# Kernel optimization log

Measured on AMD Instinct MI355X. Metric: run time of the kernel, lower is better.

## Reference

```python
import jax, jax.numpy as jnp
import numpy as np

CONFUSED_PAIRS = [(1, 2), (3, 4), (5, 6)]
NUM_CLASSES = 13
MARGIN = 0.5
IGNORE_INDEX = -100
BIG = 1e9  # finite sentinel instead of +/-inf (keeps grads clean)
EPS = 1e-12  # matches F.normalize eps

_conf_np = np.zeros((NUM_CLASSES, NUM_CLASSES), dtype=bool)
for _a, _b in CONFUSED_PAIRS:
    _conf_np[_a, _b] = True
    _conf_np[_b, _a] = True
CONF = jnp.asarray(_conf_np)  # [C, C] symmetric confused-class table


def setup_inputs() -> dict:
    key = jax.random.key(0)
    k1, k2 = jax.random.split(key)
    embeddings = jax.random.normal(k1, (16, 512, 256), dtype=jnp.float32)
    labels = jax.random.randint(k2, (16, 512), 0, 13, dtype=jnp.int64)
    return {"embeddings": embeddings, "labels": labels}


def reference(embeddings, labels):
    B, S, H = embeddings.shape
    e = embeddings.reshape(-1, H)                      # [N, H]
    lab = labels.reshape(-1)                           # [N]
    N = e.shape[0]

    valid = lab != IGNORE_INDEX                        # [N]
    # L2 normalize (F.normalize: divide by norm clamped to eps)
    norm = jnp.linalg.norm(e, axis=1, keepdims=True)
    e = e / jnp.maximum(norm, EPS)

    sim = e @ e.T                                      # [N, N] cosine sims

    lab_c = jnp.clip(lab, 0, NUM_CLASSES - 1)          # safe gather index
    # anchor label participates in some confused pair, and anchor is valid
    anchor_ok = valid & CONF[lab_c].any(axis=1)        # [N]

    same = lab[:, None] == lab[None, :]                # [N, N]
    eye = jnp.eye(N, dtype=bool)
    pos_mask = same & valid[None, :] & ~eye            # positives: same class, not self
    neg_mask = CONF[lab_c[:, None], lab_c[None, :]] & valid[None, :]  # confused-class negatives

    has_pos = pos_mask.any(axis=1)
    has_neg = neg_mask.any(axis=1)
    count_mask = anchor_ok & has_pos & has_neg         # [N] anchors contributing a triplet

    hardest_pos = jnp.min(jnp.where(pos_mask, sim, BIG), axis=1)   # [N]
    hardest_neg = jnp.max(jnp.where(neg_mask, sim, -BIG), axis=1)  # [N]

    triplet = jax.nn.relu(MARGIN + hardest_neg - hardest_pos)
    triplet = jnp.where(count_mask, triplet, 0.0)

    num_triplets = count_mask.sum()
    loss = triplet.sum() / jnp.maximum(num_triplets, 1).astype(triplet.dtype)
    return jnp.where(num_triplets > 0, loss, 0.0)
```

## Files before the change

### kernel.cpp

```cpp
#include <hip/hip_runtime.h>
#include <math.h>

#define Hdim    256
#define NMAX    8192
#define NCLS    13
#define NPADMAX (NMAX + NCLS * 32)
#define NBLK    32
#define WLMAX   264
#define NSPLIT  12
#define WPB     4
#define BIGV    1e9f
#define MARGIN  0.5f

typedef __attribute__((ext_vector_type(8))) short bf16x8;
typedef __attribute__((ext_vector_type(4))) float f32x4;

struct WS {
    unsigned short ebf[NPADMAX][Hdim];
    unsigned hpK[NPADMAX];
    unsigned hnK[NPADMAX];
    int labG[NPADMAX];
    int gpos[NMAX];
    int blockHist[NBLK][NCLS];
    int blockBase[NBLK][NCLS];
    int S[NCLS + 1];
    int n[NCLS];
    int wl_a[WLMAX];
    int wl_c[WLMAX];
    int T;
};

__device__ inline unsigned short f2bf(float f) {
    unsigned u = __float_as_uint(f);
    return (unsigned short)((u + 0x7fffu + ((u >> 16) & 1u)) >> 16);
}
__device__ inline unsigned fkey(float f) {
    unsigned u = __float_as_uint(f);
    return (u & 0x80000000u) ? ~u : (u | 0x80000000u);
}
__device__ inline float funkey(unsigned k) {
    unsigned u = (k & 0x80000000u) ? (k & 0x7fffffffu) : ~k;
    return __uint_as_float(u);
}

__global__ __launch_bounds__(256) void hist_init_kernel(const int* __restrict__ lab,
                                                        WS* ws, int N) {
    __shared__ int h[NCLS];
    int tid = threadIdx.x, b = blockIdx.x;
    if (tid < NCLS) h[tid] = 0;
    __syncthreads();
    for (int i = b * 256 + tid; i < N; i += NBLK * 256) {
        int l = lab[i];
        if (l >= 0 && l < NCLS) atomicAdd(&h[l], 1);
    }
    __syncthreads();
    if (tid < NCLS) ws->blockHist[b][tid] = h[tid];
    for (int idx = b * 256 + tid; idx < NPADMAX; idx += NBLK * 256) {
        ws->hpK[idx] = 0xFFFFFFFFu;
        ws->hnK[idx] = 0u;
        ws->labG[idx] = -1;
    }
}

__global__ __launch_bounds__(256) void plan_kernel(WS* ws) {
    __shared__ int sn[NCLS];
    int tid = threadIdx.x;
    if (tid < NCLS) {
        int s = 0;
        for (int b = 0; b < NBLK; ++b) s += ws->blockHist[b][tid];
        sn[tid] = s; ws->n[tid] = s;
    }
    __syncthreads();
    if (tid == 0) {
        int acc = 0;
        for (int c = 0; c < NCLS; ++c) { ws->S[c] = acc; acc += ((sn[c] + 31) >> 5) << 5; }
        ws->S[NCLS] = acc;
    }
    __syncthreads();
    if (tid < NCLS) {
        int base = ws->S[tid];
        for (int b = 0; b < NBLK; ++b) { ws->blockBase[b][tid] = base; base += ws->blockHist[b][tid]; }
    }
    if (tid == 0) {
        int T = 0;
        for (int c = 1; c <= 6; ++c) {
            int nt = (sn[c] + 31) >> 5;
            for (int k = 0; k < nt; ++k) { ws->wl_a[T] = ws->S[c] + 32 * k; ws->wl_c[T] = c; ++T; }
        }
        ws->T = T;
    }
}

__global__ __launch_bounds__(256) void rank_kernel(const int* __restrict__ lab,
                                                   WS* ws, int N) {
    __shared__ int cur[NCLS];
    int tid = threadIdx.x, b = blockIdx.x;
    if (tid < NCLS) cur[tid] = ws->blockBase[b][tid];
    __syncthreads();
    for (int i = b * 256 + tid; i < N; i += NBLK * 256) {
        int l = lab[i];
        int g = -1;
        if (l >= 0 && l < NCLS) g = atomicAdd(&cur[l], 1);
        ws->gpos[i] = g;
        if (g >= 0) ws->labG[g] = l;
    }
}

__global__ __launch_bounds__(256) void norm_gather_kernel(const float* __restrict__ in,
                                                          WS* ws, int N) {
    int row = blockIdx.x * 4 + (threadIdx.x >> 6);
    if (row >= N) return;
    int lane = threadIdx.x & 63;
    int g = ws->gpos[row];
    float4 v = ((const float4*)(in + (size_t)row * Hdim))[lane];
    float ss = v.x*v.x + v.y*v.y + v.z*v.z + v.w*v.w;
    #pragma unroll
    for (int off = 32; off >= 1; off >>= 1) ss += __shfl_xor(ss, off);
    float sc = 1.0f / fmaxf(sqrtf(ss), 1e-12f);
    ushort4 o;
    o.x = f2bf(v.x * sc); o.y = f2bf(v.y * sc);
    o.z = f2bf(v.z * sc); o.w = f2bf(v.w * sc);
    if (g >= 0) ((ushort4*)(&ws->ebf[g][0]))[lane] = o;
}

__global__ __launch_bounds__(256) void sim_kernel(WS* ws) {
    const int wave = threadIdx.x >> 6;
    const int lane = threadIdx.x & 63;
    const int col  = lane & 15;
    const int quad = lane >> 4;
    const int wid  = blockIdx.x * WPB + wave;
    const int tileIdx = wid / NSPLIT;
    const int split   = wid % NSPLIT;
    if (tileIdx >= ws->T) return;

    const int aBase = ws->wl_a[tileIdx];
    const int c     = ws->wl_c[tileIdx];
    const int p     = ((c - 1) ^ 1) + 1;
    const int posS = ws->S[c],  posPadE = ws->S[c + 1], posRealE = posS + ws->n[c];
    const int negS = ws->S[p],  negPadE = ws->S[p + 1], negRealE = negS + ws->n[p];
    const int nPosT = (posPadE - posS) >> 4;
    const int nT    = nPosT + ((negPadE - negS) >> 4);

    const unsigned short* ebf = &ws->ebf[0][0];

    bf16x8 afrag[2][8];
    #pragma unroll
    for (int t2 = 0; t2 < 2; ++t2) {
        const unsigned short* rp = ebf + (size_t)(aBase + t2 * 16 + col) * Hdim + quad * 8;
        #pragma unroll
        for (int ks = 0; ks < 8; ++ks)
            afrag[t2][ks] = *(const bf16x8*)(rp + ks * 32);
    }

    float runMin[2][4], runMax[2][4];
    #pragma unroll
    for (int t2 = 0; t2 < 2; ++t2)
        #pragma unroll
        for (int r = 0; r < 4; ++r) { runMin[t2][r] = BIGV; runMax[t2][r] = -BIGV; }

    auto j0Of = [&](int t) -> int {
        return (t < nPosT) ? (posS + (t << 4)) : (negS + ((t - nPosT) << 4));
    };
    bf16x8 b0[8], b1[8];
    auto loadB = [&](bf16x8 (&bf)[8], int t) {
        const unsigned short* rp = ebf + (size_t)(j0Of(t) + col) * Hdim + quad * 8;
        #pragma unroll
        for (int ks = 0; ks < 8; ++ks)
            bf[ks] = *(const bf16x8*)(rp + ks * 32);
    };
    auto computeT = [&](bf16x8 (&bf)[8], int t) {
        int j0 = j0Of(t);
        bool isPos = t < nPosT;
        int realE = isPos ? posRealE : negRealE;
        bool valid = (j0 + col) < realE;
        #pragma unroll
        for (int t2 = 0; t2 < 2; ++t2) {
            f32x4 acc = {0.f, 0.f, 0.f, 0.f};
            #pragma unroll
            for (int ks = 0; ks < 8; ++ks)
                acc = __builtin_amdgcn_mfma_f32_16x16x32_bf16(afrag[t2][ks], bf[ks], acc, 0, 0, 0);
            if (isPos) {
                #pragma unroll
                for (int r = 0; r < 4; ++r)
                    runMin[t2][r] = fminf(runMin[t2][r], valid ? acc[r] : BIGV);
            } else {
                #pragma unroll
                for (int r = 0; r < 4; ++r)
                    runMax[t2][r] = fmaxf(runMax[t2][r], valid ? acc[r] : -BIGV);
            }
        }
    };

    int nIter = (nT > split) ? ((nT - split + NSPLIT - 1) / NSPLIT) : 0;
    int t = split, i = 0;
    if (nIter > 0) loadB(b0, t);
    while (i + 2 <= nIter) {
        loadB(b1, t + NSPLIT);
        computeT(b0, t);
        if (i + 2 < nIter) loadB(b0, t + 2 * NSPLIT);
        computeT(b1, t + NSPLIT);
        t += 2 * NSPLIT; i += 2;
    }
    if (i < nIter) computeT(b0, t);

    #pragma unroll
    for (int t2 = 0; t2 < 2; ++t2)
        #pragma unroll
        for (int r = 0; r < 4; ++r) {
            float mn = runMin[t2][r], mx = runMax[t2][r];
            #pragma unroll
            for (int off = 1; off < 16; off <<= 1) {
                mn = fminf(mn, __shfl_xor(mn, off));
                mx = fmaxf(mx, __shfl_xor(mx, off));
            }
            if (col == 0) {
                int a = aBase + t2 * 16 + quad * 4 + r;
                if (mn < 1e8f)  atomicMin(&ws->hpK[a], fkey(mn));
                if (mx > -1e8f) atomicMax(&ws->hnK[a], fkey(mx));
            }
        }
}

__global__ __launch_bounds__(1024) void finalize_kernel(WS* ws, float* __restrict__ out) {
    __shared__ int ncls[NCLS];
    if (threadIdx.x < NCLS) ncls[threadIdx.x] = ws->n[threadIdx.x];
    __syncthreads();
    float sum = 0.f; int cnt = 0;
    for (int g = threadIdx.x; g < NPADMAX; g += 1024) {
        int l = ws->labG[g];
        if (l >= 1 && l <= 6) {
            int p = ((l - 1) ^ 1) + 1;
            if (ncls[l] >= 2 && ncls[p] >= 1) {
                float hp = funkey(ws->hpK[g]);
                float hn = funkey(ws->hnK[g]);
                float tr = MARGIN + hn - hp;
                if (tr > 0.f) sum += tr;
                cnt += 1;
            }
        }
    }
    #pragma unroll
    for (int off = 32; off >= 1; off >>= 1) {
        sum += __shfl_xor(sum, off);
        cnt += __shfl_xor(cnt, off);
    }
    __shared__ float ssum[16]; __shared__ int scnt[16];
    int w = threadIdx.x >> 6, lane = threadIdx.x & 63;
    if (lane == 0) { ssum[w] = sum; scnt[w] = cnt; }
    __syncthreads();
    if (threadIdx.x == 0) {
        float ts = 0.f; int tc = 0;
        #pragma unroll
        for (int k = 0; k < 16; ++k) { ts += ssum[k]; tc += scnt[k]; }
        out[0] = (tc > 0) ? ts / (float)tc : 0.f;
    }
}

extern "C" void kernel_launch(void* const* d_in, const int* in_sizes, int n_in,
                              void* d_out, int out_size, void* d_ws, size_t ws_size,
                              hipStream_t stream) {
    const float* emb = (const float*)d_in[0];
    const int*   lab = (const int*)d_in[1];
    int N = in_sizes[1];
    WS* ws = (WS*)d_ws;

    hist_init_kernel<<<NBLK, 256, 0, stream>>>(lab, ws, N);
    plan_kernel<<<1, 256, 0, stream>>>(ws);
    rank_kernel<<<NBLK, 256, 0, stream>>>(lab, ws, N);
    norm_gather_kernel<<<(N + 3) / 4, 256, 0, stream>>>(emb, ws, N);
    sim_kernel<<<(WLMAX * NSPLIT + WPB - 1) / WPB, 256, 0, stream>>>(ws);
    finalize_kernel<<<1, 1024, 0, stream>>>(ws, (float*)d_out);
}
```

Before: 103.8 us.

## Merge histogram/plan/rank into one kernel and fuse finalize into sim via last-block

Collapses the histogram, planning and ranking kernels into a single one-block kernel that only tracks classes 1-6. Normalization now skips rows with no confused class, and the finalize reduction runs inside the last finishing block of the sim kernel, found with an atomic done counter. NSPLIT rises from 12 to 16. This cuts launches from six to three and skips embedding rows that never contribute. The trade-offs are a single-block serial pass over the labels, and a norm_gather grid of N/16 that assumes N is a multiple of 16.

```diff
diff --git a/kernel.cpp b/kernel.cpp
--- a/kernel.cpp
+++ b/kernel.cpp
@@ -4,11 +4,11 @@
 #define Hdim    256
 #define NMAX    8192
 #define NCLS    13
-#define NPADMAX (NMAX + NCLS * 32)
-#define NBLK    32
+#define NPADMAX (NMAX + 6 * 32)
 #define WLMAX   264
-#define NSPLIT  12
+#define NSPLIT  16
 #define WPB     4
+#define SIMGRID ((WLMAX * NSPLIT) / WPB)
 #define BIGV    1e9f
 #define MARGIN  0.5f
 
@@ -21,13 +21,12 @@
     unsigned hnK[NPADMAX];
     int labG[NPADMAX];
     int gpos[NMAX];
-    int blockHist[NBLK][NCLS];
-    int blockBase[NBLK][NCLS];
-    int S[NCLS + 1];
-    int n[NCLS];
+    int S[8];
+    int n[8];
     int wl_a[WLMAX];
     int wl_c[WLMAX];
     int T;
+    unsigned done;
 };
 
 __device__ inline unsigned short f2bf(float f) {
@@ -43,75 +42,56 @@
     return __uint_as_float(u);
 }
 
-__global__ __launch_bounds__(256) void hist_init_kernel(const int* __restrict__ lab,
-                                                        WS* ws, int N) {
-    __shared__ int h[NCLS];
-    int tid = threadIdx.x, b = blockIdx.x;
-    if (tid < NCLS) h[tid] = 0;
-    __syncthreads();
-    for (int i = b * 256 + tid; i < N; i += NBLK * 256) {
+__global__ __launch_bounds__(1024) void plan_kernel(const int* __restrict__ lab,
+                                                    WS* ws, int N) {
+    __shared__ int h[8];
+    __shared__ int S[8];
+    __shared__ int cur[8];
+    const int tid = threadIdx.x;
+    if (tid < 8) h[tid] = 0;
+    __syncthreads();
+    for (int i = tid; i < N; i += 1024) {
         int l = lab[i];
-        if (l >= 0 && l < NCLS) atomicAdd(&h[l], 1);
-    }
-    __syncthreads();
-    if (tid < NCLS) ws->blockHist[b][tid] = h[tid];
-    for (int idx = b * 256 + tid; idx < NPADMAX; idx += NBLK * 256) {
-        ws->hpK[idx] = 0xFFFFFFFFu;
-        ws->hnK[idx] = 0u;
-        ws->labG[idx] = -1;
-    }
-}
-
-__global__ __launch_bounds__(256) void plan_kernel(WS* ws) {
-    __shared__ int sn[NCLS];
-    int tid = threadIdx.x;
-    if (tid < NCLS) {
-        int s = 0;
-        for (int b = 0; b < NBLK; ++b) s += ws->blockHist[b][tid];
-        sn[tid] = s; ws->n[tid] = s;
+        if (l >= 1 && l <= 6) atomicAdd(&h[l], 1);
     }
     __syncthreads();
     if (tid == 0) {
         int acc = 0;
-        for (int c = 0; c < NCLS; ++c) { ws->S[c] = acc; acc += ((sn[c] + 31) >> 5) << 5; }
-        ws->S[NCLS] = acc;
-    }
-    __syncthreads();
-    if (tid < NCLS) {
-        int base = ws->S[tid];
-        for (int b = 0; b < NBLK; ++b) { ws->blockBase[b][tid] = base; base += ws->blockHist[b][tid]; }
-    }
-    if (tid == 0) {
+        for (int c = 1; c <= 6; ++c) { S[c] = acc; acc += ((h[c] + 31) >> 5) << 5; }
+        S[7] = acc;
         int T = 0;
         for (int c = 1; c <= 6; ++c) {
-            int nt = (sn[c] + 31) >> 5;
-            for (int k = 0; k < nt; ++k) { ws->wl_a[T] = ws->S[c] + 32 * k; ws->wl_c[T] = c; ++T; }
+            int nt = (h[c] + 31) >> 5;
+            for (int k = 0; k < nt; ++k) { ws->wl_a[T] = S[c] + 32 * k; ws->wl_c[T] = c; ++T; }
         }
         ws->T = T;
-    }
-}
-
-__global__ __launch_bounds__(256) void rank_kernel(const int* __restrict__ lab,
-                                                   WS* ws, int N) {
-    __shared__ int cur[NCLS];
-    int tid = threadIdx.x, b = blockIdx.x;
-    if (tid < NCLS) cur[tid] = ws->blockBase[b][tid];
-    __syncthreads();
-    for (int i = b * 256 + tid; i < N; i += NBLK * 256) {
+        ws->done = 0u;
+        for (int c = 0; c < 8; ++c) { ws->n[c] = h[c]; ws->S[c] = S[c]; }
+        ws->S[7] = S[7];
+    }
+    __syncthreads();
+    const int SEnd = S[7];
+    for (int g = tid; g < SEnd; g += 1024) {
+        ws->hpK[g] = 0xFFFFFFFFu;
+        ws->hnK[g] = 0u;
+        ws->labG[g] = -1;
+    }
+    if (tid < 8) cur[tid] = S[tid];
+    __syncthreads();
+    for (int i = tid; i < N; i += 1024) {
         int l = lab[i];
         int g = -1;
-        if (l >= 0 && l < NCLS) g = atomicAdd(&cur[l], 1);
+        if (l >= 1 && l <= 6) { g = atomicAdd(&cur[l], 1); ws->labG[g] = l; }
         ws->gpos[i] = g;
-        if (g >= 0) ws->labG[g] = l;
-    }
-}
-
-__global__ __launch_bounds__(256) void norm_gather_kernel(const float* __restrict__ in,
-                                                          WS* ws, int N) {
-    int row = blockIdx.x * 4 + (threadIdx.x >> 6);
-    if (row >= N) return;
+    }
+}
+
+__global__ __launch_bounds__(1024) void norm_gather_kernel(const float* __restrict__ in,
+                                                           WS* ws) {
+    int row  = blockIdx.x * 16 + (threadIdx.x >> 6);
     int lane = threadIdx.x & 63;
     int g = ws->gpos[row];
+    if (g < 0) return;
     float4 v = ((const float4*)(in + (size_t)row * Hdim))[lane];
     float ss = v.x*v.x + v.y*v.y + v.z*v.z + v.w*v.w;
     #pragma unroll
@@ -120,10 +100,10 @@
     ushort4 o;
     o.x = f2bf(v.x * sc); o.y = f2bf(v.y * sc);
     o.z = f2bf(v.z * sc); o.w = f2bf(v.w * sc);
-    if (g >= 0) ((ushort4*)(&ws->ebf[g][0]))[lane] = o;
-}
-
-__global__ __launch_bounds__(256) void sim_kernel(WS* ws) {
+    ((ushort4*)(&ws->ebf[g][0]))[lane] = o;
+}
+
+__global__ __launch_bounds__(256) void sim_kernel(WS* ws, float* __restrict__ out) {
     const int wave = threadIdx.x >> 6;
     const int lane = threadIdx.x & 63;
     const int col  = lane & 15;
@@ -131,104 +111,119 @@
     const int wid  = blockIdx.x * WPB + wave;
     const int tileIdx = wid / NSPLIT;
     const int split   = wid % NSPLIT;
-    if (tileIdx >= ws->T) return;
-
-    const int aBase = ws->wl_a[tileIdx];
-    const int c     = ws->wl_c[tileIdx];
-    const int p     = ((c - 1) ^ 1) + 1;
-    const int posS = ws->S[c],  posPadE = ws->S[c + 1], posRealE = posS + ws->n[c];
-    const int negS = ws->S[p],  negPadE = ws->S[p + 1], negRealE = negS + ws->n[p];
-    const int nPosT = (posPadE - posS) >> 4;
-    const int nT    = nPosT + ((negPadE - negS) >> 4);
-
-    const unsigned short* ebf = &ws->ebf[0][0];
-
-    bf16x8 afrag[2][8];
-    #pragma unroll
-    for (int t2 = 0; t2 < 2; ++t2) {
-        const unsigned short* rp = ebf + (size_t)(aBase + t2 * 16 + col) * Hdim + quad * 8;
-        #pragma unroll
-        for (int ks = 0; ks < 8; ++ks)
-            afrag[t2][ks] = *(const bf16x8*)(rp + ks * 32);
-    }
-
-    float runMin[2][4], runMax[2][4];
-    #pragma unroll
-    for (int t2 = 0; t2 < 2; ++t2)
-        #pragma unroll
-        for (int r = 0; r < 4; ++r) { runMin[t2][r] = BIGV; runMax[t2][r] = -BIGV; }
-
-    auto j0Of = [&](int t) -> int {
-        return (t < nPosT) ? (posS + (t << 4)) : (negS + ((t - nPosT) << 4));
-    };
-    bf16x8 b0[8], b1[8];
-    auto loadB = [&](bf16x8 (&bf)[8], int t) {
-        const unsigned short* rp = ebf + (size_t)(j0Of(t) + col) * Hdim + quad * 8;
-        #pragma unroll
-        for (int ks = 0; ks < 8; ++ks)
-            bf[ks] = *(const bf16x8*)(rp + ks * 32);
-    };
-    auto computeT = [&](bf16x8 (&bf)[8], int t) {
-        int j0 = j0Of(t);
-        bool isPos = t < nPosT;
-        int realE = isPos ? posRealE : negRealE;
-        bool valid = (j0 + col) < realE;
+
+    if (tileIdx < ws->T) {
+        const int aBase = ws->wl_a[tileIdx];
+        const int c     = ws->wl_c[tileIdx];
+        const int p     = ((c - 1) ^ 1) + 1;
+        const int posS = ws->S[c], posRealE = posS + ws->n[c];
+        const int negS = ws->S[p], negRealE = negS + ws->n[p];
+        const int nPosT = (ws->S[c + 1] - posS) >> 4;
+        const int nT    = nPosT + ((((p == c + 1) ? ws->S[p + 1] : ws->S[p])
+                                    - negS) >> 4);
+        const int nNegT = ((ws->S[p + 1]) - negS) >> 4;
+        const int nTT = nPosT + nNegT;
+
+        const unsigned short* ebf = &ws->ebf[0][0];
+
+        bf16x8 afrag[2][8];
         #pragma unroll
         for (int t2 = 0; t2 < 2; ++t2) {
-            f32x4 acc = {0.f, 0.f, 0.f, 0.f};
+            const unsigned short* rp = ebf + (size_t)(aBase + t2 * 16 + col) * Hdim + quad * 8;
             #pragma unroll
             for (int ks = 0; ks < 8; ++ks)
-                acc = __builtin_amdgcn_mfma_f32_16x16x32_bf16(afrag[t2][ks], bf[ks], acc, 0, 0, 0);
-            if (isPos) {
+                afrag[t2][ks] = *(const bf16x8*)(rp + ks * 32);
+        }
+
+        float runMin[2][4], runMax[2][4];
+        #pragma unroll
+        for (int t2 = 0; t2 < 2; ++t2)
+            #pragma unroll
+            for (int r = 0; r < 4; ++r) { runMin[t2][r] = BIGV; runMax[t2][r] = -BIGV; }
+
+        auto j0Of = [&](int t) -> int {
+            return (t < nPosT) ? (posS + (t << 4)) : (negS + ((t - nPosT) << 4));
+        };
+        bf16x8 b0[8], b1[8];
+        auto loadB = [&](bf16x8 (&bf)[8], int t) {
+            const unsigned short* rp = ebf + (size_t)(j0Of(t) + col) * Hdim + quad * 8;
+            #pragma unroll
+            for (int ks = 0; ks < 8; ++ks)
+                bf[ks] = *(const bf16x8*)(rp + ks * 32);
+        };
+        auto computeT = [&](bf16x8 (&bf)[8], int t) {
+            int j0 = j0Of(t);
+            bool isPos = t < nPosT;
+            int realE  = isPos ? posRealE : negRealE;
+            bool valid = (j0 + col) < realE;
+            #pragma unroll
+            for (int t2 = 0; t2 < 2; ++t2) {
+                f32x4 acc = {0.f, 0.f, 0.f, 0.f};
                 #pragma unroll
-                for (int r = 0; r < 4; ++r)
-                    runMin[t2][r] = fminf(runMin[t2][r], valid ? acc[r] : BIGV);
-            } else {
+                for (int ks = 0; ks < 8; ++ks)
+                    acc = __builtin_amdgcn_mfma_f32_16x16x32_bf16(afrag[t2][ks], bf[ks], acc, 0, 0, 0);
+                if (isPos) {
+                    #pragma unroll
+                    for (int r = 0; r < 4; ++r)
+                        runMin[t2][r] = fminf(runMin[t2][r], valid ? acc[r] : BIGV);
+                } else {
+                    #pragma unroll
+                    for (int r = 0; r < 4; ++r)
+                        runMax[t2][r] = fmaxf(runMax[t2][r], valid ? acc[r] : -BIGV);
+                }
+            }
+        };
+
+        int nIter = (nTT > split) ? ((nTT - split + NSPLIT - 1) / NSPLIT) : 0;
+        int t = split, i = 0;
+        if (nIter > 0) loadB(b0, t);
+        while (i + 2 <= nIter) {
+            loadB(b1, t + NSPLIT);
+            computeT(b0, t);
+            if (i + 2 < nIter) loadB(b0, t + 2 * NSPLIT);
+            computeT(b1, t + NSPLIT);
+            t += 2 * NSPLIT; i += 2;
+        }
+        if (i < nIter) computeT(b0, t);
+        (void)nT;
+
+        #pragma unroll
+        for (int t2 = 0; t2 < 2; ++t2)
+            #pragma unroll
+            for (int r = 0; r < 4; ++r) {
+                float mn = runMin[t2][r], mx = runMax[t2][r];
                 #pragma unroll
-                for (int r = 0; r < 4; ++r)
-                    runMax[t2][r] = fmaxf(runMax[t2][r], valid ? acc[r] : -BIGV);
+                for (int off = 1; off < 16; off <<= 1) {
+                    mn = fminf(mn, __shfl_xor(mn, off));
+                    mx = fmaxf(mx, __shfl_xor(mx, off));
+                }
+                if (col == 0) {
+                    int a = aBase + t2 * 16 + quad * 4 + r;
+                    if (mn < 1e8f)  atomicMin(&ws->hpK[a], fkey(mn));
+                    if (mx > -1e8f) atomicMax(&ws->hnK[a], fkey(mx));
+                }
             }
-        }
-    };
-
-    int nIter = (nT > split) ? ((nT - split + NSPLIT - 1) / NSPLIT) : 0;
-    int t = split, i = 0;
-    if (nIter > 0) loadB(b0, t);
-    while (i + 2 <= nIter) {
-        loadB(b1, t + NSPLIT);
-        computeT(b0, t);
-        if (i + 2 < nIter) loadB(b0, t + 2 * NSPLIT);
-        computeT(b1, t + NSPLIT);
-        t += 2 * NSPLIT; i += 2;
-    }
-    if (i < nIter) computeT(b0, t);
-
-    #pragma unroll
-    for (int t2 = 0; t2 < 2; ++t2)
-        #pragma unroll
-        for (int r = 0; r < 4; ++r) {
-            float mn = runMin[t2][r], mx = runMax[t2][r];
-            #pragma unroll
-            for (int off = 1; off < 16; off <<= 1) {
-                mn = fminf(mn, __shfl_xor(mn, off));
-                mx = fmaxf(mx, __shfl_xor(mx, off));
-            }
-            if (col == 0) {
-                int a = aBase + t2 * 16 + quad * 4 + r;
-                if (mn < 1e8f)  atomicMin(&ws->hpK[a], fkey(mn));
-                if (mx > -1e8f) atomicMax(&ws->hnK[a], fkey(mx));
-            }
-        }
-}
-
-__global__ __launch_bounds__(1024) void finalize_kernel(WS* ws, float* __restrict__ out) {
-    __shared__ int ncls[NCLS];
-    if (threadIdx.x < NCLS) ncls[threadIdx.x] = ws->n[threadIdx.x];
+    }
+
+    __shared__ int isLast;
+    __syncthreads();
+    if (threadIdx.x == 0) {
+        __threadfence();
+        unsigned old = atomicAdd(&ws->done, 1u);
+        isLast = (old == (unsigned)(gridDim.x - 1)) ? 1 : 0;
+    }
+    __syncthreads();
+    if (!isLast) return;
+    __threadfence();
+
+    __shared__ int ncls[8];
+    if (threadIdx.x < 8) ncls[threadIdx.x] = ws->n[threadIdx.x];
     __syncthreads();
     float sum = 0.f; int cnt = 0;
-    for (int g = threadIdx.x; g < NPADMAX; g += 1024) {
+    const int SEnd = ws->S[7];
+    for (int g = threadIdx.x; g < SEnd; g += 256) {
         int l = ws->labG[g];
-        if (l >= 1 && l <= 6) {
+        if (l >= 1) {
             int p = ((l - 1) ^ 1) + 1;
             if (ncls[l] >= 2 && ncls[p] >= 1) {
                 float hp = funkey(ws->hpK[g]);
@@ -244,14 +239,13 @@
         sum += __shfl_xor(sum, off);
         cnt += __shfl_xor(cnt, off);
     }
-    __shared__ float ssum[16]; __shared__ int scnt[16];
-    int w = threadIdx.x >> 6, lane = threadIdx.x & 63;
-    if (lane == 0) { ssum[w] = sum; scnt[w] = cnt; }
+    __shared__ float ssum[4]; __shared__ int scnt[4];
+    int w = threadIdx.x >> 6;
+    if ((threadIdx.x & 63) == 0) { ssum[w] = sum; scnt[w] = cnt; }
     __syncthreads();
     if (threadIdx.x == 0) {
-        float ts = 0.f; int tc = 0;
-        #pragma unroll
-        for (int k = 0; k < 16; ++k) { ts += ssum[k]; tc += scnt[k]; }
+        float ts = ssum[0] + ssum[1] + ssum[2] + ssum[3];
+        int   tc = scnt[0] + scnt[1] + scnt[2] + scnt[3];
         out[0] = (tc > 0) ? ts / (float)tc : 0.f;
     }
 }
@@ -264,10 +258,7 @@
     int N = in_sizes[1];
     WS* ws = (WS*)d_ws;
 
-    hist_init_kernel<<<NBLK, 256, 0, stream>>>(lab, ws, N);
-    plan_kernel<<<1, 256, 0, stream>>>(ws);
-    rank_kernel<<<NBLK, 256, 0, stream>>>(lab, ws, N);
-    norm_gather_kernel<<<(N + 3) / 4, 256, 0, stream>>>(emb, ws, N);
-    sim_kernel<<<(WLMAX * NSPLIT + WPB - 1) / WPB, 256, 0, stream>>>(ws);
-    finalize_kernel<<<1, 1024, 0, stream>>>(ws, (float*)d_out);
-}
+    plan_kernel<<<1, 1024, 0, stream>>>(lab, ws, N);
+    norm_gather_kernel<<<N / 16, 1024, 0, stream>>>(emb, ws);
+    sim_kernel<<<SIMGRID, 256, 0, stream>>>(ws, (float*)d_out);
+}
```

Result: slower. 111.3 us (+7.3%).
